# Optimization experiments

Measured on AMD Instinct MI355X. Metric: run time of the kernel, lower is better.

## Reference

```python
import jax, jax.numpy as jnp
import numpy as np

K = 20           # top_k
EPS_NORM = 1e-12  # F.normalize default eps


def setup_inputs() -> dict:
    key = jax.random.key(0)
    ks = jax.random.split(key, 16)
    B, C, R, S, SCB, ST, H = 8192, 3755, 214, 13, 30, 6, 64
    return {
        "char_logits": jax.random.normal(ks[0], (B, C), jnp.float32),
        "radical_logits": jax.random.normal(ks[1], (B, R), jnp.float32),
        "structure": jax.random.normal(ks[2], (B, S), jnp.float32),
        "stroke_count": jax.random.normal(ks[3], (B, SCB), jnp.float32),
        "stroke_types": jax.random.normal(ks[4], (B, ST), jnp.float32),
        "radical_mask": jax.random.randint(ks[5], (C, R), 0, 2, jnp.int32),
        "structure_label": jax.random.randint(ks[6], (C,), 0, S, jnp.int32),
        "stroke_count_label": jax.random.randint(ks[7], (C,), 0, SCB, jnp.int32),
        "stroke_type_sig": jax.random.uniform(ks[8], (C, ST), jnp.float32),
        "W1": jax.random.normal(ks[9], (6, H), jnp.float32) * 0.3,
        "b1": jax.random.normal(ks[10], (H,), jnp.float32) * 0.1,
        "W2": jax.random.normal(ks[11], (H, 1), jnp.float32) * 0.3,
        "b2": jax.random.normal(ks[12], (1,), jnp.float32) * 0.1,
        "reranker_weight": jnp.asarray(0.1, jnp.float32),
    }


def _features(char_logits, radical_logits, structure, stroke_count, stroke_types,
              radical_mask, structure_label, stroke_count_label, stroke_type_sig,
              top_idx):
    sg = jax.lax.stop_gradient
    # all model outputs except char_logits are detached by caller; char_logits
    # is detached inside _compute_features for the neural-confidence feature
    rl, st, sc, sty = sg(radical_logits), sg(structure), sg(stroke_count), sg(stroke_types)
    cl_d = sg(char_logits)

    # feature 1/2: radical match & false-alarm ratios
    radical_probs = jax.nn.sigmoid(rl)                              # (B, R)
    cand_mask = radical_mask[top_idx].astype(jnp.float32)           # (B, K, R)
    detected = jnp.einsum('br,bkr->bk', radical_probs, cand_mask)   # (B, K)
    cand_counts = jnp.maximum(cand_mask.sum(-1), 1.0)
    radical_match_ratio = detected / cand_counts
    total_prob = jnp.maximum(radical_probs.sum(-1, keepdims=True), 1e-6)  # (B,1)
    false_alarm_mass = radical_probs.sum(-1, keepdims=True) - detected
    radical_false_ratio = false_alarm_mass / total_prob

    # feature 3: structure match probability
    structure_probs = jax.nn.softmax(st, axis=-1)                   # (B, S)
    cand_structure = structure_label[top_idx]                       # (B, K)
    structure_match = jnp.take_along_axis(structure_probs, cand_structure, axis=1)

    # feature 4: normalized stroke-count distance
    stroke_pred = jnp.argmax(sc, axis=-1)                           # (B,)
    cand_stroke = stroke_count_label[top_idx]                       # (B, K)
    stroke_distance = jnp.abs(stroke_pred[:, None] - cand_stroke).astype(jnp.float32) / 29.0

    # feature 5: zero-masked stroke-type cosine
    cand_sig = stroke_type_sig[top_idx]                             # (B, K, 6)
    sig_norm_val = jnp.linalg.norm(cand_sig, axis=-1)               # (B, K)
    has_sig = (sig_norm_val > 1e-6).astype(jnp.float32)
    pred_norm = sty / jnp.maximum(jnp.linalg.norm(sty, axis=-1, keepdims=True), EPS_NORM)
    cand_adj = cand_sig + 1e-8 * (1.0 - has_sig)[..., None]
    cand_norm = cand_adj / jnp.maximum(jnp.linalg.norm(cand_adj, axis=-1, keepdims=True), EPS_NORM)
    stroke_type_cos = jnp.einsum('bd,bkd->bk', pred_norm, cand_norm) * has_sig

    # feature 6: detached neural confidence
    neural_probs = jax.nn.softmax(cl_d, axis=-1)                    # (B, C)
    neural_conf = jnp.take_along_axis(neural_probs, top_idx, axis=1)

    return jnp.stack([radical_match_ratio, radical_false_ratio, structure_match,
                      stroke_distance, stroke_type_cos, neural_conf], axis=-1)  # (B, K, 6)


def reference(char_logits, radical_logits, structure, stroke_count, stroke_types,
              radical_mask, structure_label, stroke_count_label, stroke_type_sig,
              W1, b1, W2, b2, reranker_weight):
    B = char_logits.shape[0]
    top_logits, top_idx = jax.lax.top_k(char_logits, K)             # (B, K)
    feats = _features(char_logits, radical_logits, structure, stroke_count,
                      stroke_types, radical_mask, structure_label,
                      stroke_count_label, stroke_type_sig, top_idx)
    h = jax.nn.relu(feats @ W1 + b1)                                # (B, K, H)
    rerank_scores = (h @ W2 + b2)[..., 0]                           # (B, K)
    combined_top = top_logits + reranker_weight * rerank_scores
    rows = jnp.arange(B)[:, None]
    return char_logits.at[rows, top_idx].set(combined_top)
```

## Files before the change

kernel.cpp:

```cpp
#include <hip/hip_runtime.h>
#include <math.h>

#define NB   8192
#define NC   3755
#define NR   214
#define NS   13
#define NSC  30
#define NST  6
#define NH   64
#define KTOP 20
#define RPB  4
#define NT   (RPB * 64)
#define NQT  15
#define NBIN 1024
#define CAP  192

__device__ __forceinline__ unsigned sortkey(float x) {
    unsigned u = __float_as_uint(x);
    return (u & 0x80000000u) ? ~u : (u | 0x80000000u);
}
__device__ __forceinline__ float inv_sortkey(unsigned k) {
    unsigned u = (k & 0x80000000u) ? (k ^ 0x80000000u) : ~k;
    return __uint_as_float(u);
}

__global__ __launch_bounds__(NT, 8) void select_kernel(
    const float* __restrict__ char_logits,
    float*       __restrict__ out,
    float*       __restrict__ ws_topv,
    int*         __restrict__ ws_topi,
    float*       __restrict__ ws_stat)
{
    const int tid  = threadIdx.x;
    const int lane = tid & 63;
    const int wave = tid >> 6;
    const int row  = blockIdx.x * RPB + wave;

    __shared__ unsigned           s_hist32[RPB / 2][NBIN];
    __shared__ unsigned long long s_cand[RPB][CAP];
    __shared__ int s_cnt[RPB];
    __shared__ int s_need[RPB];

    const int      hw  = wave >> 1;
    const unsigned hsh = (wave & 1) * 16;

    const size_t rowOff = (size_t)row * NC;
    const float* __restrict__ rin  = char_logits + rowOff;
    float*       __restrict__ rout = out + rowOff;

    const int a     = (int)((4 - (rowOff & 3)) & 3);
    const int nq    = (NC - a) >> 2;
    const int ntail = NC - a - 4 * nq;

    int ext_idx = -1;
    if (lane < a)                           ext_idx = lane;
    else if (lane >= 8 && lane < 8 + ntail) ext_idx = a + 4 * nq + (lane - 8);

    if (tid < RPB) s_cnt[tid] = 0;
    __syncthreads();

    const unsigned FLOORK = 0xC0000000u;
    float m0 = -INFINITY, m1 = -INFINITY, m2 = -INFINITY, m3 = -INFINITY;
    float e0 = 0.f, e1 = 0.f, e2 = 0.f, e3 = 0.f;
    float ext = -INFINITY;
    if (ext_idx >= 0) {
        ext = rin[ext_idx]; rout[ext_idx] = ext;
        e0 += __expf(ext);
        m0 = fmaxf(m0, ext);
        unsigned k = sortkey(ext);
        if (k >= FLOORK) {
            int pos = atomicAdd(&s_cnt[wave], 1);
            if (pos < CAP)
                s_cand[wave][pos] = ((unsigned long long)k << 32) | (0xFFFFFFFFu - (unsigned)ext_idx);
        }
    }
    for (int t = 0; t < NQT; ++t) {
        int q = lane + t * 64;
        if (q < nq) {
            float4 x = *reinterpret_cast<const float4*>(rin + a + 4 * q);
            *reinterpret_cast<float4*>(rout + a + 4 * q) = x;
            e0 += __expf(x.x); e1 += __expf(x.y);
            e2 += __expf(x.z); e3 += __expf(x.w);
            m0 = fmaxf(m0, x.x); m1 = fmaxf(m1, x.y);
            m2 = fmaxf(m2, x.z); m3 = fmaxf(m3, x.w);
            unsigned kk[4] = { sortkey(x.x), sortkey(x.y), sortkey(x.z), sortkey(x.w) };
#pragma unroll
            for (int j = 0; j < 4; ++j) {
                if (kk[j] >= FLOORK) {
                    int pos = atomicAdd(&s_cnt[wave], 1);
                    if (pos < CAP)
                        s_cand[wave][pos] = ((unsigned long long)kk[j] << 32)
                                          | (0xFFFFFFFFu - (unsigned)(a + 4*q + j));
                }
            }
        }
    }
    float lmax = fmaxf(fmaxf(m0, m1), fmaxf(m2, m3));
#pragma unroll
    for (int off = 32; off > 0; off >>= 1) lmax = fmaxf(lmax, __shfl_xor(lmax, off));
    const float rowmax = lmax;
    float S = (e0 + e1) + (e2 + e3);
#pragma unroll
    for (int off = 32; off > 0; off >>= 1) S += __shfl_xor(S, off);

    int M = s_cnt[wave];
    const bool ok = (M >= KTOP) && (M <= CAP) && (fabsf(rowmax) <= 60.f);
    float sumexp = S * __expf(-rowmax);
    if (lane == 0) s_need[wave] = ok ? 0 : 1;
    __syncthreads();
    const int any = s_need[0] | s_need[1] | s_need[2] | s_need[3];

    if (any) {
        const bool bad = !ok;
        for (int i = tid; i < (RPB / 2) * NBIN; i += NT)
            (&s_hist32[0][0])[i] = 0u;
        __syncthreads();
        if (bad) {
            if (ext_idx >= 0) atomicAdd(&s_hist32[hw][sortkey(ext) >> 22], 1u << hsh);
            for (int t = 0; t < NQT; ++t) {
                int q = lane + t * 64;
                if (q < nq) {
                    float4 x = *reinterpret_cast<const float4*>(rin + a + 4 * q);
                    atomicAdd(&s_hist32[hw][sortkey(x.x) >> 22], 1u << hsh);
                    atomicAdd(&s_hist32[hw][sortkey(x.y) >> 22], 1u << hsh);
                    atomicAdd(&s_hist32[hw][sortkey(x.z) >> 22], 1u << hsh);
                    atomicAdd(&s_hist32[hw][sortkey(x.w) >> 22], 1u << hsh);
                }
            }
        }
        __syncthreads();
        int B0 = 0;
        if (bad) {
            int bb = (int)(sortkey(rowmax) >> 22), cum = 0;
            while (bb >= 0) {
                cum += (int)((s_hist32[hw][bb] >> hsh) & 0xFFFFu);
                if (cum >= KTOP) break;
                --bb;
            }
            B0 = (bb < 0) ? 0 : bb;
            if (lane == 0) s_cnt[wave] = 0;
        }
        __syncthreads();
        if (bad) {
            float f0 = 0.f, f1 = 0.f, f2 = 0.f, f3 = 0.f;
            if (ext_idx >= 0) {
                f0 += __expf(ext - rowmax);
                unsigned k = sortkey(ext);
                if ((int)(k >> 22) >= B0) {
                    int pos = atomicAdd(&s_cnt[wave], 1);
                    if (pos < CAP)
                        s_cand[wave][pos] = ((unsigned long long)k << 32) | (0xFFFFFFFFu - (unsigned)ext_idx);
                }
            }
            for (int t = 0; t < NQT; ++t) {
                int q = lane + t * 64;
                if (q < nq) {
                    float4 x = *reinterpret_cast<const float4*>(rin + a + 4 * q);
                    f0 += __expf(x.x - rowmax); f1 += __expf(x.y - rowmax);
                    f2 += __expf(x.z - rowmax); f3 += __expf(x.w - rowmax);
                    unsigned kk[4] = { sortkey(x.x), sortkey(x.y), sortkey(x.z), sortkey(x.w) };
#pragma unroll
                    for (int j = 0; j < 4; ++j) {
                        if ((int)(kk[j] >> 22) >= B0) {
                            int pos = atomicAdd(&s_cnt[wave], 1);
                            if (pos < CAP)
                                s_cand[wave][pos] = ((unsigned long long)kk[j] << 32)
                                                  | (0xFFFFFFFFu - (unsigned)(a + 4*q + j));
                        }
                    }
                }
            }
            float ls = (f0 + f1) + (f2 + f3);
#pragma unroll
            for (int off = 32; off > 0; off >>= 1) ls += __shfl_xor(ls, off);
            sumexp = ls;
            M = s_cnt[wave]; if (M > CAP) M = CAP;
        }
    }

    for (int c = lane; c < M; c += 64) {
        unsigned long long pc = s_cand[wave][c];
        int rank = 0;
        for (int j = 0; j < M; ++j) rank += (s_cand[wave][j] > pc) ? 1 : 0;
        if (rank < KTOP) {
            ws_topv[(size_t)row * KTOP + rank] = inv_sortkey((unsigned)(pc >> 32));
            ws_topi[(size_t)row * KTOP + rank] = (int)(0xFFFFFFFFu - (unsigned)(pc & 0xFFFFFFFFu));
        }
    }
    if (lane == 0) {
        ws_stat[2 * row + 0] = rowmax;
        ws_stat[2 * row + 1] = sumexp;
    }
}

__global__ __launch_bounds__(256, 8) void rerank_kernel(
    const float* __restrict__ radical_logits,
    const float* __restrict__ structure,
    const float* __restrict__ stroke_count,
    const float* __restrict__ stroke_types,
    const int*   __restrict__ radical_mask,
    const int*   __restrict__ structure_label,
    const int*   __restrict__ stroke_count_label,
    const float* __restrict__ stroke_type_sig,
    const float* __restrict__ W1,
    const float* __restrict__ b1,
    const float* __restrict__ W2,
    const float* __restrict__ b2,
    const float* __restrict__ rw,
    const float* __restrict__ ws_topv,
    const int*   __restrict__ ws_topi,
    const float* __restrict__ ws_stat,
    float*       __restrict__ out)
{
    const int row  = blockIdx.x;
    const int tid  = threadIdx.x;
    const int lane = tid & 63;
    const int wave = tid >> 6;

    __shared__ float s_probs[216];
    __shared__ float s_struct[NS];
    __shared__ float s_aux[8];
    __shared__ float s_topv[KTOP];
    __shared__ int   s_topi[KTOP];
    __shared__ float s_stat2[2];

    if (tid < NR)
        s_probs[tid] = 1.f / (1.f + __expf(-radical_logits[(size_t)row * NR + tid]));
    if (tid < KTOP) {
        s_topv[tid] = ws_topv[(size_t)row * KTOP + tid];
        s_topi[tid] = ws_topi[(size_t)row * KTOP + tid];
    }
    if (tid == 216) {
        float sv[NS]; float m = -INFINITY;
#pragma unroll
        for (int i = 0; i < NS; ++i) { sv[i] = structure[(size_t)row * NS + i]; m = fmaxf(m, sv[i]); }
        float s = 0.f;
#pragma unroll
        for (int i = 0; i < NS; ++i) { sv[i] = __expf(sv[i] - m); s += sv[i]; }
        float inv = 1.f / s;
#pragma unroll
        for (int i = 0; i < NS; ++i) s_struct[i] = sv[i] * inv;
    } else if (tid == 217) {
        float bv = -INFINITY; int bi = 0;
#pragma unroll
        for (int i = 0; i < NSC; ++i) {
            float x = stroke_count[(size_t)row * NSC + i];
            if (x > bv) { bv = x; bi = i; }
        }
        s_aux[6] = (float)bi;
    } else if (tid == 218) {
        float t6[NST]; float ss = 0.f;
#pragma unroll
        for (int i = 0; i < NST; ++i) { t6[i] = stroke_types[(size_t)row * NST + i]; ss += t6[i] * t6[i]; }
        float inv = 1.f / fmaxf(sqrtf(ss), 1e-12f);
#pragma unroll
        for (int i = 0; i < NST; ++i) s_aux[i] = t6[i] * inv;
    } else if (tid == 219) {
        s_stat2[0] = ws_stat[2 * row + 0];
        s_stat2[1] = ws_stat[2 * row + 1];
    }
    __syncthreads();

    float psum = 0.f;
#pragma unroll
    for (int i = 0; i < 4; ++i) {
        int r = lane + i * 64;
        if (r < NR) psum += s_probs[r];
    }
#pragma unroll
    for (int off = 32; off > 0; off >>= 1) psum += __shfl_xor(psum, off);
    const float total = psum;

    const float rowmax = s_stat2[0];
    const float sumexp = s_stat2[1];
    const float b1v = b1[lane];
    float w1v[6];
#pragma unroll
    for (int j = 0; j < 6; ++j) w1v[j] = W1[j * NH + lane];
    const float w2v = W2[lane];
    const float b2v = b2[0];
    const float wrk = rw[0];
    const float spred = s_aux[6];

#pragma unroll
    for (int j = 0; j < KTOP / 4; ++j) {
        const int   k  = wave * (KTOP / 4) + j;
        const int   ci = __builtin_amdgcn_readfirstlane(s_topi[k]);
        const float tv = s_topv[k];
        const int* __restrict__ mrow = radical_mask + (size_t)ci * NR;
        float det = 0.f, cnt = 0.f;
#pragma unroll
        for (int i = 0; i < 4; ++i) {
            int r = lane + i * 64;
            if (r < NR) {
                float m = (float)mrow[r];
                det += s_probs[r] * m;
                cnt += m;
            }
        }
#pragma unroll
        for (int off = 32; off > 0; off >>= 1) {
            det += __shfl_xor(det, off);
            cnt += __shfl_xor(cnt, off);
        }
        float f1 = det / fmaxf(cnt, 1.f);
        float f2 = (total - det) / fmaxf(total, 1e-6f);
        float f3 = s_struct[structure_label[ci]];
        float f4 = fabsf(spred - (float)stroke_count_label[ci]) * (1.f / 29.f);
        float sig[NST]; float ss = 0.f;
#pragma unroll
        for (int i = 0; i < NST; ++i) { sig[i] = stroke_type_sig[(size_t)ci * NST + i]; ss += sig[i] * sig[i]; }
        float nrm = sqrtf(ss);
        float has = (nrm > 1e-6f) ? 1.f : 0.f;
        float add = 1e-8f * (1.f - has);
        float ss2 = 0.f;
#pragma unroll
        for (int i = 0; i < NST; ++i) { sig[i] += add; ss2 += sig[i] * sig[i]; }
        float inv = 1.f / fmaxf(sqrtf(ss2), 1e-12f);
        float dot = 0.f;
#pragma unroll
        for (int i = 0; i < NST; ++i) dot += s_aux[i] * sig[i] * inv;
        float f5 = dot * has;
        float f6 = __expf(tv - rowmax) / sumexp;

        float acc = b1v + f1 * w1v[0] + f2 * w1v[1] + f3 * w1v[2]
                        + f4 * w1v[3] + f5 * w1v[4] + f6 * w1v[5];
        float h = fmaxf(acc, 0.f);
        float part = h * w2v;
#pragma unroll
        for (int off = 32; off > 0; off >>= 1) part += __shfl_xor(part, off);
        if (lane == 0) out[(size_t)row * NC + ci] = tv + wrk * (part + b2v);
    }
}

extern "C" void kernel_launch(void* const* d_in, const int* in_sizes, int n_in,
                              void* d_out, int out_size, void* d_ws, size_t ws_size,
                              hipStream_t stream) {
    (void)in_sizes; (void)n_in; (void)out_size; (void)ws_size;
    const float* char_logits        = (const float*)d_in[0];
    const float* radical_logits     = (const float*)d_in[1];
    const float* structure          = (const float*)d_in[2];
    const float* stroke_count       = (const float*)d_in[3];
    const float* stroke_types       = (const float*)d_in[4];
    const int*   radical_mask       = (const int*)d_in[5];
    const int*   structure_label    = (const int*)d_in[6];
    const int*   stroke_count_label = (const int*)d_in[7];
    const float* stroke_type_sig    = (const float*)d_in[8];
    const float* W1                 = (const float*)d_in[9];
    const float* b1                 = (const float*)d_in[10];
    const float* W2                 = (const float*)d_in[11];
    const float* b2                 = (const float*)d_in[12];
    const float* rw                 = (const float*)d_in[13];
    float* out = (float*)d_out;

    float* ws_topv = (float*)d_ws;
    int*   ws_topi = (int*)(ws_topv + (size_t)NB * KTOP);
    float* ws_stat = (float*)(ws_topi + (size_t)NB * KTOP);

    select_kernel<<<NB / RPB, NT, 0, stream>>>(char_logits, out, ws_topv, ws_topi, ws_stat);
    rerank_kernel<<<NB, 256, 0, stream>>>(
        radical_logits, structure, stroke_count, stroke_types,
        radical_mask, structure_label, stroke_count_label, stroke_type_sig,
        W1, b1, W2, b2, rw, ws_topv, ws_topi, ws_stat, out);
}
```

Baseline: 343.7 us.

## Bit-pack radical mask, ballot-compact candidates, nontemporal copy stores

Adds a prep kernel that packs each character's 214-int radical mask into 256 bits. The rerank kernel then reads 32 bytes per candidate instead of about 856 and computes the match count with popcount and lane-bit tests. In the select kernel, the per-element shared atomics for candidate collection become wave ballot plus mbcnt prefix compaction. The copy loop is unrolled with a peeled tail and uses nontemporal stores for the output. The costs are an extra kernel launch, extra workspace, and a rewritten candidate path. The fallback path still uses s_cnt, which is no longer zeroed on the fast path.

```diff
diff --git a/kernel.cpp b/kernel.cpp
--- a/kernel.cpp
+++ b/kernel.cpp
@@ -15,6 +15,8 @@
 #define NBIN 1024
 #define CAP  192
 
+typedef float __attribute__((ext_vector_type(4))) f32x4;
+
 __device__ __forceinline__ unsigned sortkey(float x) {
     unsigned u = __float_as_uint(x);
     return (u & 0x80000000u) ? ~u : (u | 0x80000000u);
@@ -22,6 +24,35 @@
 __device__ __forceinline__ float inv_sortkey(unsigned k) {
     unsigned u = (k & 0x80000000u) ? (k ^ 0x80000000u) : ~k;
     return __uint_as_float(u);
+}
+__device__ __forceinline__ int lane_prefix(unsigned long long m) {
+    int c = __builtin_amdgcn_mbcnt_lo((unsigned)m, 0);
+    return __builtin_amdgcn_mbcnt_hi((unsigned)(m >> 32), c);
+}
+
+__global__ __launch_bounds__(256) void prep_kernel(
+    const int* __restrict__ radical_mask,
+    unsigned*  __restrict__ ws_bits)
+{
+    const int lane = threadIdx.x & 63;
+    const int wave = threadIdx.x >> 6;
+    const int c    = blockIdx.x * 4 + wave;
+    if (c >= NC) return;
+    unsigned long long bits[4];
+#pragma unroll
+    for (int i = 0; i < 4; ++i) {
+        int r = lane + i * 64;
+        bool pred = (r < NR) && (radical_mask[(size_t)c * NR + r] != 0);
+        bits[i] = __ballot(pred);
+    }
+    if (lane == 0) {
+        uint4 wa = make_uint4((unsigned)bits[0], (unsigned)(bits[0] >> 32),
+                              (unsigned)bits[1], (unsigned)(bits[1] >> 32));
+        uint4 wb = make_uint4((unsigned)bits[2], (unsigned)(bits[2] >> 32),
+                              (unsigned)bits[3], (unsigned)(bits[3] >> 32));
+        reinterpret_cast<uint4*>(ws_bits)[(size_t)c * 2 + 0] = wa;
+        reinterpret_cast<uint4*>(ws_bits)[(size_t)c * 2 + 1] = wb;
+    }
 }
 
 __global__ __launch_bounds__(NT, 8) void select_kernel(
@@ -56,45 +87,80 @@
     if (lane < a)                           ext_idx = lane;
     else if (lane >= 8 && lane < 8 + ntail) ext_idx = a + 4 * nq + (lane - 8);
 
-    if (tid < RPB) s_cnt[tid] = 0;
-    __syncthreads();
-
     const unsigned FLOORK = 0xC0000000u;
-    float m0 = -INFINITY, m1 = -INFINITY, m2 = -INFINITY, m3 = -INFINITY;
-    float e0 = 0.f, e1 = 0.f, e2 = 0.f, e3 = 0.f;
     float ext = -INFINITY;
     if (ext_idx >= 0) {
-        ext = rin[ext_idx]; rout[ext_idx] = ext;
-        e0 += __expf(ext);
-        m0 = fmaxf(m0, ext);
+        ext = rin[ext_idx];
+        __builtin_nontemporal_store(ext, rout + ext_idx);
+    }
+    float e0 = __expf(ext), e1 = 0.f, e2 = 0.f, e3 = 0.f;
+    float m0 = ext, m1 = -INFINITY, m2 = -INFINITY, m3 = -INFINITY;
+    int base = 0;
+
+#pragma unroll
+    for (int t = 0; t < 14; ++t) {
+        const int q = lane + t * 64;
+        float4 x = *reinterpret_cast<const float4*>(rin + a + 4 * q);
+        f32x4 v = { x.x, x.y, x.z, x.w };
+        __builtin_nontemporal_store(v, reinterpret_cast<f32x4*>(rout + a + 4 * q));
+        e0 += __expf(x.x); e1 += __expf(x.y);
+        e2 += __expf(x.z); e3 += __expf(x.w);
+        m0 = fmaxf(m0, x.x); m1 = fmaxf(m1, x.y);
+        m2 = fmaxf(m2, x.z); m3 = fmaxf(m3, x.w);
+        unsigned kk[4] = { sortkey(x.x), sortkey(x.y), sortkey(x.z), sortkey(x.w) };
+#pragma unroll
+        for (int j = 0; j < 4; ++j) {
+            bool pred = kk[j] >= FLOORK;
+            unsigned long long bal = __ballot(pred);
+            if (pred) {
+                int pos = base + lane_prefix(bal);
+                if (pos < CAP)
+                    s_cand[wave][pos] = ((unsigned long long)kk[j] << 32)
+                                      | (0xFFFFFFFFu - (unsigned)(a + 4 * q + j));
+            }
+            base += (int)__popcll(bal);
+        }
+    }
+    {
+        const int q = lane + 896;
+        const bool inb = q < nq;
+        float4 x = make_float4(-INFINITY, -INFINITY, -INFINITY, -INFINITY);
+        if (inb) {
+            x = *reinterpret_cast<const float4*>(rin + a + 4 * q);
+            f32x4 v = { x.x, x.y, x.z, x.w };
+            __builtin_nontemporal_store(v, reinterpret_cast<f32x4*>(rout + a + 4 * q));
+        }
+        e0 += __expf(x.x); e1 += __expf(x.y);
+        e2 += __expf(x.z); e3 += __expf(x.w);
+        m0 = fmaxf(m0, x.x); m1 = fmaxf(m1, x.y);
+        m2 = fmaxf(m2, x.z); m3 = fmaxf(m3, x.w);
+        unsigned kk[4] = { sortkey(x.x), sortkey(x.y), sortkey(x.z), sortkey(x.w) };
+#pragma unroll
+        for (int j = 0; j < 4; ++j) {
+            bool pred = kk[j] >= FLOORK;
+            unsigned long long bal = __ballot(pred);
+            if (pred) {
+                int pos = base + lane_prefix(bal);
+                if (pos < CAP)
+                    s_cand[wave][pos] = ((unsigned long long)kk[j] << 32)
+                                      | (0xFFFFFFFFu - (unsigned)(a + 4 * q + j));
+            }
+            base += (int)__popcll(bal);
+        }
+    }
+    {
         unsigned k = sortkey(ext);
-        if (k >= FLOORK) {
-            int pos = atomicAdd(&s_cnt[wave], 1);
+        bool pred = k >= FLOORK;
+        unsigned long long bal = __ballot(pred);
+        if (pred) {
+            int pos = base + lane_prefix(bal);
             if (pos < CAP)
-                s_cand[wave][pos] = ((unsigned long long)k << 32) | (0xFFFFFFFFu - (unsigned)ext_idx);
-        }
-    }
-    for (int t = 0; t < NQT; ++t) {
-        int q = lane + t * 64;
-        if (q < nq) {
-            float4 x = *reinterpret_cast<const float4*>(rin + a + 4 * q);
-            *reinterpret_cast<float4*>(rout + a + 4 * q) = x;
-            e0 += __expf(x.x); e1 += __expf(x.y);
-            e2 += __expf(x.z); e3 += __expf(x.w);
-            m0 = fmaxf(m0, x.x); m1 = fmaxf(m1, x.y);
-            m2 = fmaxf(m2, x.z); m3 = fmaxf(m3, x.w);
-            unsigned kk[4] = { sortkey(x.x), sortkey(x.y), sortkey(x.z), sortkey(x.w) };
-#pragma unroll
-            for (int j = 0; j < 4; ++j) {
-                if (kk[j] >= FLOORK) {
-                    int pos = atomicAdd(&s_cnt[wave], 1);
-                    if (pos < CAP)
-                        s_cand[wave][pos] = ((unsigned long long)kk[j] << 32)
-                                          | (0xFFFFFFFFu - (unsigned)(a + 4*q + j));
-                }
-            }
-        }
-    }
+                s_cand[wave][pos] = ((unsigned long long)k << 32)
+                                  | (0xFFFFFFFFu - (unsigned)ext_idx);
+        }
+        base += (int)__popcll(bal);
+    }
+
     float lmax = fmaxf(fmaxf(m0, m1), fmaxf(m2, m3));
 #pragma unroll
     for (int off = 32; off > 0; off >>= 1) lmax = fmaxf(lmax, __shfl_xor(lmax, off));
@@ -103,7 +169,7 @@
 #pragma unroll
     for (int off = 32; off > 0; off >>= 1) S += __shfl_xor(S, off);
 
-    int M = s_cnt[wave];
+    int M = base;
     const bool ok = (M >= KTOP) && (M <= CAP) && (fabsf(rowmax) <= 60.f);
     float sumexp = S * __expf(-rowmax);
     if (lane == 0) s_need[wave] = ok ? 0 : 1;
@@ -165,7 +231,7 @@
                             int pos = atomicAdd(&s_cnt[wave], 1);
                             if (pos < CAP)
                                 s_cand[wave][pos] = ((unsigned long long)kk[j] << 32)
-                                                  | (0xFFFFFFFFu - (unsigned)(a + 4*q + j));
+                                                  | (0xFFFFFFFFu - (unsigned)(a + 4 * q + j));
                         }
                     }
                 }
@@ -198,7 +264,6 @@
     const float* __restrict__ structure,
     const float* __restrict__ stroke_count,
     const float* __restrict__ stroke_types,
-    const int*   __restrict__ radical_mask,
     const int*   __restrict__ structure_label,
     const int*   __restrict__ stroke_count_label,
     const float* __restrict__ stroke_type_sig,
@@ -210,6 +275,7 @@
     const float* __restrict__ ws_topv,
     const int*   __restrict__ ws_topi,
     const float* __restrict__ ws_stat,
+    const unsigned* __restrict__ ws_bits,
     float*       __restrict__ out)
 {
     const int row  = blockIdx.x;
@@ -217,15 +283,15 @@
     const int lane = tid & 63;
     const int wave = tid >> 6;
 
-    __shared__ float s_probs[216];
+    __shared__ float s_probs[256];
     __shared__ float s_struct[NS];
     __shared__ float s_aux[8];
     __shared__ float s_topv[KTOP];
     __shared__ int   s_topi[KTOP];
     __shared__ float s_stat2[2];
 
-    if (tid < NR)
-        s_probs[tid] = 1.f / (1.f + __expf(-radical_logits[(size_t)row * NR + tid]));
+    s_probs[tid] = (tid < NR)
+        ? 1.f / (1.f + __expf(-radical_logits[(size_t)row * NR + tid])) : 0.f;
     if (tid < KTOP) {
         s_topv[tid] = ws_topv[(size_t)row * KTOP + tid];
         s_topi[tid] = ws_topi[(size_t)row * KTOP + tid];
@@ -261,12 +327,11 @@
     }
     __syncthreads();
 
-    float psum = 0.f;
-#pragma unroll
-    for (int i = 0; i < 4; ++i) {
-        int r = lane + i * 64;
-        if (r < NR) psum += s_probs[r];
-    }
+    const float p0 = s_probs[lane];
+    const float p1 = s_probs[lane + 64];
+    const float p2 = s_probs[lane + 128];
+    const float p3 = s_probs[lane + 192];
+    float psum = p0 + p1 + p2 + p3;
 #pragma unroll
     for (int off = 32; off > 0; off >>= 1) psum += __shfl_xor(psum, off);
     const float total = psum;
@@ -281,28 +346,27 @@
     const float b2v = b2[0];
     const float wrk = rw[0];
     const float spred = s_aux[6];
+    const unsigned l5 = lane & 31;
+    const bool hi = lane >= 32;
 
 #pragma unroll
     for (int j = 0; j < KTOP / 4; ++j) {
         const int   k  = wave * (KTOP / 4) + j;
         const int   ci = __builtin_amdgcn_readfirstlane(s_topi[k]);
         const float tv = s_topv[k];
-        const int* __restrict__ mrow = radical_mask + (size_t)ci * NR;
-        float det = 0.f, cnt = 0.f;
-#pragma unroll
-        for (int i = 0; i < 4; ++i) {
-            int r = lane + i * 64;
-            if (r < NR) {
-                float m = (float)mrow[r];
-                det += s_probs[r] * m;
-                cnt += m;
-            }
-        }
-#pragma unroll
-        for (int off = 32; off > 0; off >>= 1) {
-            det += __shfl_xor(det, off);
-            cnt += __shfl_xor(cnt, off);
-        }
+
+        const uint4* bq = reinterpret_cast<const uint4*>(ws_bits) + (size_t)ci * 2;
+        const uint4 wa = bq[0], wb = bq[1];
+        float cnt = (float)(__popc(wa.x) + __popc(wa.y) + __popc(wa.z) + __popc(wa.w)
+                          + __popc(wb.x) + __popc(wb.y) + __popc(wb.z));
+        float det = 0.f;
+        det += ((( hi ? wa.y : wa.x) >> l5) & 1u) ? p0 : 0.f;
+        det += ((( hi ? wa.w : wa.z) >> l5) & 1u) ? p1 : 0.f;
+        det += ((( hi ? wb.y : wb.x) >> l5) & 1u) ? p2 : 0.f;
+        det += ((( hi ? wb.w : wb.z) >> l5) & 1u) ? p3 : 0.f;
+#pragma unroll
+        for (int off = 32; off > 0; off >>= 1) det += __shfl_xor(det, off);
+
         float f1 = det / fmaxf(cnt, 1.f);
         float f2 = (total - det) / fmaxf(total, 1e-6f);
         float f3 = s_struct[structure_label[ci]];
@@ -353,13 +417,15 @@
     const float* rw                 = (const float*)d_in[13];
     float* out = (float*)d_out;
 
-    float* ws_topv = (float*)d_ws;
-    int*   ws_topi = (int*)(ws_topv + (size_t)NB * KTOP);
-    float* ws_stat = (float*)(ws_topi + (size_t)NB * KTOP);
-
+    float*    ws_topv = (float*)d_ws;
+    int*      ws_topi = (int*)(ws_topv + (size_t)NB * KTOP);
+    float*    ws_stat = (float*)(ws_topi + (size_t)NB * KTOP);
+    unsigned* ws_bits = (unsigned*)(ws_stat + (size_t)NB * 2);
+
+    prep_kernel<<<(NC + 3) / 4, 256, 0, stream>>>(radical_mask, ws_bits);
     select_kernel<<<NB / RPB, NT, 0, stream>>>(char_logits, out, ws_topv, ws_topi, ws_stat);
     rerank_kernel<<<NB, 256, 0, stream>>>(
         radical_logits, structure, stroke_count, stroke_types,
-        radical_mask, structure_label, stroke_count_label, stroke_type_sig,
-        W1, b1, W2, b2, rw, ws_topv, ws_topi, ws_stat, out);
-}
+        structure_label, stroke_count_label, stroke_type_sig,
+        W1, b1, W2, b2, rw, ws_topv, ws_topi, ws_stat, ws_bits, out);
+}
```

Measured after the change: 381.6 us. 1.11x slower.
